# Optimization experiments

Measured on AMD Instinct MI355X. Metric: run time of the kernel, lower is better.

Reference implementation:

```python
import jax, jax.numpy as jnp
import numpy as np

TEMP = 1.0
PONDER_COST = 0.01
HALT_BIAS = 0.0


def _layernorm(x, g, b, eps=1e-5):
    mu = x.mean(-1, keepdims=True)
    var = ((x - mu) ** 2).mean(-1, keepdims=True)
    return (x - mu) * jax.lax.rsqrt(var + eps) * g + b


def _bank_forward_all(x, w1, b1, w2, b2):
    # x: [B,N,H] -> every expert's output [B,N,E,H]
    h = jax.nn.relu(jnp.einsum('bnh,ehf->bnef', x, w1) + b1)  # [B,N,E,F]
    return jnp.einsum('bnef,efh->bneh', h, w2) + b2


def setup_inputs() -> dict:
    key = jax.random.key(0)
    ks = jax.random.split(key, 10)
    B, N, H, E, F = 8, 2048, 256, 32, 512
    inv_h = 1.0 / np.sqrt(H).astype(np.float32)
    inv_f = 1.0 / np.sqrt(F).astype(np.float32)
    n = lambda k, s, sc: jax.random.normal(k, s, jnp.float32) * sc
    return {
        'tokens_in': n(ks[0], (B, N, H), 1.0),
        'Wp': n(ks[1], (H, H), inv_h), 'bp': jnp.zeros((H,), jnp.float32),
        'Wq1': n(ks[2], (H, H), inv_h), 'Wq2': n(ks[3], (H, H), inv_h),
        'keys_e': n(ks[4], (E, H), inv_h),  # torch: randn/sqrt(H)
        'transition_bias': jnp.zeros((E, E), jnp.float32),
        'halt_ln_g': jnp.ones((H,), jnp.float32), 'halt_ln_b': jnp.zeros((H,), jnp.float32),
        'halt_w': n(ks[5], (H, 1), inv_h), 'halt_b': jnp.zeros((1,), jnp.float32),
        'w1': n(ks[6], (E, H, F), inv_h), 'b1': jnp.zeros((E, F), jnp.float32),
        'w2': n(ks[7], (E, F, H), inv_f), 'b2': jnp.zeros((E, H), jnp.float32),
        'norm_g': jnp.ones((H,), jnp.float32), 'norm_b': jnp.zeros((H,), jnp.float32),
    }


def reference(tokens_in, Wp, bp, Wq1, Wq2, keys_e, transition_bias,
              halt_ln_g, halt_ln_b, halt_w, halt_b,
              w1, b1, w2, b2, norm_g, norm_b):
    H = tokens_in.shape[-1]
    scale = 1.0 / jnp.sqrt(jnp.asarray(H, tokens_in.dtype))
    tokens = tokens_in @ Wp + bp                       # input_proj [B,N,H]

    # hop 1: query-key routing + full expert bank + softmax mix
    scores_1 = ((tokens @ Wq1) @ keys_e.T) * scale     # [B,N,E]
    probs_1 = jax.nn.softmax(scores_1 / TEMP, axis=-1)
    out_1 = _bank_forward_all(tokens, w1, b1, w2, b2)  # [B,N,E,H]
    hop_1 = jnp.einsum('bneh,bne->bnh', out_1, probs_1)
    top1_idx = jnp.argmax(probs_1, axis=-1)            # [B,N]

    # halting head
    halt_prob = jax.nn.sigmoid(_layernorm(hop_1, halt_ln_g, halt_ln_b) @ halt_w + halt_b + HALT_BIAS)  # [B,N,1]

    # hop 2 with transition bias from hop-1 top expert
    scores_2 = ((hop_1 @ Wq2) @ keys_e.T) * scale + transition_bias[top1_idx]
    probs_2 = jax.nn.softmax(scores_2 / TEMP, axis=-1)
    out_2 = _bank_forward_all(hop_1, w1, b1, w2, b2)
    hop_2 = jnp.einsum('bneh,bne->bnh', out_2, probs_2)

    continue_prob = 1.0 - halt_prob
    mixed = halt_prob * hop_1 + continue_prob * hop_2
    tokens_out = _layernorm(tokens + mixed, norm_g, norm_b)
    pooled = tokens_out.mean(axis=1)                   # masked_mean (no mask)
    ponder_loss = continue_prob.mean() * PONDER_COST
    return pooled, tokens_out, ponder_loss
```

## Files before the change

### kernel.cpp

```cpp
#include <hip/hip_runtime.h>

typedef short short8 __attribute__((ext_vector_type(8)));
typedef float f32x4 __attribute__((ext_vector_type(4)));

#define MFMA16(a, b, c) __builtin_amdgcn_mfma_f32_16x16x32_bf16(a, b, c, 0, 0, 0)

static __device__ __forceinline__ unsigned pk2(float a, float b) {
  unsigned r;
  asm("v_cvt_pk_bf16_f32 %0, %1, %2" : "=v"(r) : "v"(a), "v"(b));
  return r;
}
static __device__ __forceinline__ float bf2f(unsigned short u) {
  union { unsigned u; float f; } v; v.u = ((unsigned)u) << 16; return v.f;
}
static __device__ __forceinline__ void async16(void* lds, const void* g) {
  __builtin_amdgcn_global_load_lds(
      (const __attribute__((address_space(1))) unsigned*)g,
      (__attribute__((address_space(3))) unsigned*)lds, 16, 0, 0);
}
static __device__ __forceinline__ float wsum64(float v) {
#pragma unroll
  for (int m = 1; m < 64; m <<= 1) v += __shfl_xor(v, m);
  return v;
}

#define LOAD4(B, P)                                   \
  {                                                   \
    const unsigned short* _p = (P);                   \
    B[0] = *(const short8*)(_p);                      \
    B[1] = *(const short8*)(_p + 512);                \
    B[2] = *(const short8*)(_p + 1024);               \
    B[3] = *(const short8*)(_p + 1536);               \
  }

__global__ void k_prep(const float* __restrict__ w1, const float* __restrict__ w2,
                       const float* __restrict__ Wp, const float* __restrict__ Wq1,
                       const float* __restrict__ Wq2, const float* __restrict__ keys,
                       unsigned short* __restrict__ w1f, unsigned short* __restrict__ w2f,
                       unsigned short* __restrict__ wpt, float* __restrict__ wk1,
                       float* __restrict__ wk2, float* __restrict__ dout) {
  __shared__ __align__(16) short T[64 * 266];
  const int b = blockIdx.x, tid = threadIdx.x;
  if (b < 512) {
    int e = b >> 4, fq = (b >> 2) & 3, kc = b & 3;
    const float* src = w1 + (e * 256 + kc * 64) * 512 + fq * 128;
    for (int c = tid; c < 1024; c += 256) {
      int hr = c >> 4, c8 = c & 15;
      const float* s = src + hr * 512 + c8 * 8;
      f32x4 v0 = *(const f32x4*)s;
      f32x4 v1 = *(const f32x4*)(s + 4);
      unsigned* tp = (unsigned*)(T + hr * 138 + c8 * 8);
      tp[0] = pk2(v0.x, v0.y); tp[1] = pk2(v0.z, v0.w);
      tp[2] = pk2(v1.x, v1.y); tp[3] = pk2(v1.z, v1.w);
    }
    __syncthreads();
#pragma unroll
    for (int j = 0; j < 4; ++j) {
      int o = tid + j * 256;
      int fl = o >> 3, k8 = o & 7;
      unsigned qq[4];
#pragma unroll
      for (int p = 0; p < 4; ++p) {
        unsigned a0 = (unsigned short)T[(k8 * 8 + p * 2) * 138 + fl];
        unsigned a1 = (unsigned short)T[(k8 * 8 + p * 2 + 1) * 138 + fl];
        qq[p] = a0 | (a1 << 16);
      }
      uint4 q; q.x = qq[0]; q.y = qq[1]; q.z = qq[2]; q.w = qq[3];
      int set = kc * 2 + (k8 >> 2);
      int lane = (k8 & 3) * 16 + (fl & 15);
      int wvf = fl >> 6, fr = (fl >> 4) & 3;
      *(uint4*)(w1f + (size_t)(e * 4 + fq) * 32768 + set * 4096 + wvf * 2048 + fr * 512 +
                lane * 8) = q;
    }
  } else if (b < 768) {
    int b2 = b - 512;
    int e = b2 >> 3, fq = (b2 >> 1) & 3, kcc = b2 & 1;
    const float* src = w2 + (e * 512 + fq * 128 + kcc * 64) * 256;
    for (int c = tid; c < 2048; c += 256) {
      int fr = c >> 5, c8 = c & 31;
      const float* s = src + fr * 256 + c8 * 8;
      f32x4 v0 = *(const f32x4*)s;
      f32x4 v1 = *(const f32x4*)(s + 4);
      unsigned* tp = (unsigned*)(T + fr * 266 + c8 * 8);
      tp[0] = pk2(v0.x, v0.y); tp[1] = pk2(v0.z, v0.w);
      tp[2] = pk2(v1.x, v1.y); tp[3] = pk2(v1.z, v1.w);
    }
    __syncthreads();
#pragma unroll
    for (int j = 0; j < 8; ++j) {
      int o = tid + j * 256;
      int hd = o >> 3, k8 = o & 7;
      unsigned qq[4];
#pragma unroll
      for (int p = 0; p < 4; ++p) {
        unsigned a0 = (unsigned short)T[(k8 * 8 + p * 2) * 266 + hd];
        unsigned a1 = (unsigned short)T[(k8 * 8 + p * 2 + 1) * 266 + hd];
        qq[p] = a0 | (a1 << 16);
      }
      uint4 q; q.x = qq[0]; q.y = qq[1]; q.z = qq[2]; q.w = qq[3];
      int kc2 = kcc * 2 + (k8 >> 2);
      int lane = (k8 & 3) * 16 + (hd & 15);
      *(uint4*)(w2f + (size_t)(e * 4 + fq) * 32768 + kc2 * 8192 + (hd >> 4) * 512 +
                lane * 8) = q;
    }
  } else if (b < 776) {
    int b3 = b - 768;
    int fq = b3 >> 2, kc = b3 & 3;
    const float* src = Wp + (kc * 64) * 256 + fq * 128;
    for (int c = tid; c < 1024; c += 256) {
      int hr = c >> 4, c8 = c & 15;
      const float* s = src + hr * 256 + c8 * 8;
      f32x4 v0 = *(const f32x4*)s;
      f32x4 v1 = *(const f32x4*)(s + 4);
      unsigned* tp = (unsigned*)(T + hr * 138 + c8 * 8);
      tp[0] = pk2(v0.x, v0.y); tp[1] = pk2(v0.z, v0.w);
      tp[2] = pk2(v1.x, v1.y); tp[3] = pk2(v1.z, v1.w);
    }
    __syncthreads();
#pragma unroll
    for (int j = 0; j < 4; ++j) {
      int o = tid + j * 256;
      int fl = o >> 3, k8 = o & 7;
      unsigned qq[4];
#pragma unroll
      for (int p = 0; p < 4; ++p) {
        unsigned a0 = (unsigned short)T[(k8 * 8 + p * 2) * 138 + fl];
        unsigned a1 = (unsigned short)T[(k8 * 8 + p * 2 + 1) * 138 + fl];
        qq[p] = a0 | (a1 << 16);
      }
      uint4 q; q.x = qq[0]; q.y = qq[1]; q.z = qq[2]; q.w = qq[3];
      int off = (fl * 64 + k8 * 8) ^ ((fl & 7) << 3);
      *(uint4*)(wpt + b3 * 8192 + off) = q;
    }
  } else if (b < 792) {
    int b4 = b - 776;
    const float* Wq = (b4 >= 8) ? Wq2 : Wq1;
    float* Wk = (b4 >= 8) ? wk2 : wk1;
    const int kb = (b4 & 7) * 32;
    float* KT = (float*)T;
    for (int i = tid; i < 8192; i += 256) {
      int e = i >> 8, j = i & 255;
      KT[j * 32 + ((e + j) & 31)] = keys[e * 256 + j];
    }
    __syncthreads();
    const int e = tid & 31, kk = (tid >> 5) * 2;
    f32x4 acc0 = (f32x4)(0.0f), acc1 = (f32x4)(0.0f);
    const float* wq0 = Wq + (size_t)(kb + kk) * 256;
#pragma unroll 4
    for (int j = 0; j < 256; j += 4) {
      f32x4 kt;
      kt.x = KT[j * 32 + ((e + j) & 31)];
      kt.y = KT[(j + 1) * 32 + ((e + j + 1) & 31)];
      kt.z = KT[(j + 2) * 32 + ((e + j + 2) & 31)];
      kt.w = KT[(j + 3) * 32 + ((e + j + 3) & 31)];
      acc0 += *(const f32x4*)(wq0 + j) * kt;
      acc1 += *(const f32x4*)(wq0 + 256 + j) * kt;
    }
    Wk[(kb + kk) * 32 + e] = acc0.x + acc0.y + acc0.z + acc0.w;
    Wk[(kb + kk + 1) * 32 + e] = acc1.x + acc1.y + acc1.z + acc1.w;
  } else {
    for (int i = tid; i < 2048; i += 256) dout[i] = 0.0f;
    if (tid == 0) dout[2048 + 4194304] = 0.0f;
  }
}

#define P_LDS_W 67584
#define P_LDS_BP 100352
#define P_LDS_TOT 101376

__launch_bounds__(512, 2)
__global__ void k_proj(const float* __restrict__ xin, const unsigned short* __restrict__ wpt,
                       const float* __restrict__ bp, float* __restrict__ tokf,
                       unsigned short* __restrict__ tokb) {
  extern __shared__ char smem[];
  const int tid = threadIdx.x;
  const int tb = blockIdx.x * 128;
  const int w = tid >> 6, l = tid & 63, l15 = l & 15, l4 = l >> 4;

  for (int s = tid; s < 4096; s += 512) {
    int row = s >> 5, c8 = s & 31;
    const float* src = xin + (tb + row) * 256 + c8 * 8;
    f32x4 v0 = *(const f32x4*)src;
    f32x4 v1 = *(const f32x4*)(src + 4);
    uint4 pv;
    pv.x = pk2(v0.x, v0.y); pv.y = pk2(v0.z, v0.w);
    pv.z = pk2(v1.x, v1.y); pv.w = pk2(v1.z, v1.w);
    *(uint4*)(smem + row * 528 + c8 * 16) = pv;
  }
  if (tid < 256) ((float*)(smem + P_LDS_BP))[tid] = bp[tid];
  __syncthreads();

  const int wv_f = w >> 2, wv_t = w & 3;
  for (int fq = 0; fq < 2; ++fq) {
    f32x4 acc[8];
#pragma unroll
    for (int i = 0; i < 8; ++i) acc[i] = (f32x4)(0.0f);
    const char* cbase = (const char*)(wpt + (fq * 4) * 8192);
    {
      char* dst = smem + P_LDS_W;
      async16(dst + w * 2048, cbase + w * 2048 + l * 16);
      async16(dst + w * 2048 + 1024, cbase + w * 2048 + 1024 + l * 16);
    }
    __syncthreads();
    for (int kc = 0; kc < 4; ++kc) {
      int cur = kc & 1;
      if (kc < 3) {
        char* dst = smem + P_LDS_W + (cur ^ 1) * 16384;
        const char* src = cbase + (kc + 1) * 16384;
        async16(dst + w * 2048, src + w * 2048 + l * 16);
        async16(dst + w * 2048 + 1024, src + w * 2048 + 1024 + l * 16);
      }
      const char* Wc = smem + P_LDS_W + cur * 16384;
#pragma unroll
      for (int ks = 0; ks < 2; ++ks) {
        short8 af[4], bfr[2];
#pragma unroll
        for (int fr = 0; fr < 4; ++fr) {
          int frow = wv_f * 64 + fr * 16 + l15;
          int off = (frow * 128 + ks * 64 + l4 * 16) ^ ((frow & 7) << 4);
          af[fr] = *(const short8*)(Wc + off);
        }
#pragma unroll
        for (int tf = 0; tf < 2; ++tf) {
          int tok = wv_t * 32 + tf * 16 + l15;
          bfr[tf] = *(const short8*)(smem + tok * 528 + kc * 128 + ks * 64 + l4 * 16);
        }
#pragma unroll
        for (int fr = 0; fr < 4; ++fr)
#pragma unroll
          for (int tf = 0; tf < 2; ++tf)
            acc[fr * 2 + tf] = MFMA16(af[fr], bfr[tf], acc[fr * 2 + tf]);
      }
      __syncthreads();
    }
    const float* BP = (const float*)(smem + P_LDS_BP);
#pragma unroll
    for (int fr = 0; fr < 4; ++fr) {
      int hd0 = fq * 128 + wv_f * 64 + fr * 16 + l4 * 4;
      f32x4 bv = *(const f32x4*)(BP + hd0);
#pragma unroll
      for (int tf = 0; tf < 2; ++tf) {
        int tok = tb + wv_t * 32 + tf * 16 + l15;
        f32x4 o = acc[fr * 2 + tf] + bv;
        *(f32x4*)(tokf + tok * 256 + hd0) = o;
        uint2 hv; hv.x = pk2(o.x, o.y); hv.y = pk2(o.z, o.w);
        *(uint2*)(tokb + tok * 256 + hd0) = hv;
      }
    }
  }
}

__global__ void k_router1(const float* __restrict__ tokf, const float* __restrict__ wk1,
                          float* __restrict__ probs1, int* __restrict__ top1) {
  __shared__ float WK[8192];
  const int tid = threadIdx.x;
  for (int i = tid; i < 8192; i += 256) WK[i] = wk1[i];
  __syncthreads();
  const int w = tid >> 6, l = tid & 63;
  const int e = l & 31, half = l >> 5;
  for (int tt = 0; tt < 16; ++tt) {
    int t = blockIdx.x * 64 + w * 16 + tt;
    const float* row = tokf + t * 256 + half * 128;
    const float* wkh = WK + half * 128 * 32 + e;
    float s = 0.f;
    for (int kk = 0; kk < 128; ++kk) s += row[kk] * wkh[kk * 32];
    s += __shfl_xor(s, 32);
    s *= 0.0625f;
    float m = s;
#pragma unroll
    for (int off = 16; off > 0; off >>= 1) m = fmaxf(m, __shfl_xor(m, off, 32));
    float ex = __expf(s - m);
    float sum = ex;
#pragma unroll
    for (int off = 16; off > 0; off >>= 1) sum += __shfl_xor(sum, off, 32);
    if (l < 32) probs1[t * 32 + e] = ex / sum;
    float bs = s; int bi = e;
#pragma unroll
    for (int off = 16; off > 0; off >>= 1) {
      float os = __shfl_xor(bs, off, 32);
      int oi = __shfl_xor(bi, off, 32);
      if (os > bs || (os == bs && oi < bi)) { bs = os; bi = oi; }
    }
    if (l == 0) top1[t] = bi;
  }
}

#define B_PR 65536
#define B_B1 73728
#define B_TOT 106496

__launch_bounds__(512, 2)
__global__ void k_bank(const unsigned short* __restrict__ xg, const float* __restrict__ probsg,
                       const float* __restrict__ b1g, const unsigned short* __restrict__ w1f,
                       const unsigned short* __restrict__ w2f, float* __restrict__ partg) {
  extern __shared__ char smem[];
  const int tid = threadIdx.x;
  const int xcd = blockIdx.x & 7;
  const int grp = xcd >> 2;
  const int tile = (xcd & 3) * 32 + (blockIdx.x >> 3);
  const int tb = tile * 128;
  const int w = tid >> 6, l = tid & 63, l15 = l & 15, l4 = l >> 4;
  const int wv_f = w >> 2, wv_t = w & 3;
  const int wv_h = w >> 1, wv_t2 = w & 1;
  float* PRL = (float*)(smem + B_PR);
  float* B1L = (float*)(smem + B_B1);

  for (int s = tid; s < 2048; s += 512)
    PRL[s] = probsg[(size_t)(tb + (s & 127)) * 32 + grp * 16 + (s >> 7)];
  for (int s = tid; s < 8192; s += 512) B1L[s] = b1g[grp * 8192 + s];

  short8 xr[16];
#pragma unroll
  for (int tf = 0; tf < 2; ++tf)
#pragma unroll
    for (int kc = 0; kc < 4; ++kc)
#pragma unroll
      for (int ks = 0; ks < 2; ++ks) {
        int tok = tb + wv_t * 32 + tf * 16 + l15;
        xr[tf * 8 + kc * 2 + ks] =
            *(const short8*)(xg + (size_t)tok * 256 + kc * 64 + ks * 32 + l4 * 8);
      }
  __syncthreads();

  const unsigned short* w1e = w1f + (size_t)grp * 64 * 32768;
  const unsigned short* w2e = w2f + (size_t)grp * 64 * 32768;
  const int o1 = wv_f * 2048 + l * 8;
  const int o2 = wv_h * 2048 + l * 8;

  f32x4 acc2[16];
#pragma unroll
  for (int i = 0; i < 16; ++i) acc2[i] = (f32x4)(0.0f);

  short8 wb[3][4];
  LOAD4(wb[0], w1e + 0 * 4096 + o1);
  LOAD4(wb[1], w1e + 1 * 4096 + o1);
  int hcur = 0;

  for (int el = 0; el < 64; ++el) {
    const unsigned short* w1c = w1e + (size_t)el * 32768;
    const unsigned short* w2c = w2e + (size_t)el * 32768;
    const int e = el >> 2, fq = el & 3;

    f32x4 acc1[8];
#pragma unroll
    for (int i = 0; i < 8; ++i) acc1[i] = (f32x4)(0.0f);
#pragma unroll
    for (int k = 0; k < 8; ++k) {
      if (k < 6) { LOAD4(wb[(k + 2) % 3], w1c + (k + 2) * 4096 + o1); }
      else       { LOAD4(wb[(k + 2) % 3], w2c + (k - 6) * 8192 + o2); }
      __builtin_amdgcn_s_setprio(1);
#pragma unroll
      for (int fr = 0; fr < 4; ++fr)
#pragma unroll
        for (int tf = 0; tf < 2; ++tf)
          acc1[fr * 2 + tf] = MFMA16(wb[k % 3][fr], xr[tf * 8 + k], acc1[fr * 2 + tf]);
      __builtin_amdgcn_s_setprio(0);
    }

    {
      const float* bb = B1L + e * 512 + fq * 128;
      const float* pp = PRL + e * 128;
      float p0 = pp[wv_t * 32 + l15];
      float p1 = pp[wv_t * 32 + 16 + l15];
      char* Hw = smem + hcur * 32768;
#pragma unroll
      for (int fr = 0; fr < 4; ++fr) {
        int f0 = wv_f * 64 + fr * 16 + l4 * 4;
        f32x4 bvv = *(const f32x4*)(bb + f0);
#pragma unroll
        for (int tf = 0; tf < 2; ++tf) {
          int tok = wv_t * 32 + tf * 16 + l15;
          float p = tf ? p1 : p0;
          f32x4 a = acc1[fr * 2 + tf];
          float h0 = fmaxf(a.x + bvv.x, 0.f) * p;
          float h1 = fmaxf(a.y + bvv.y, 0.f) * p;
          float h2 = fmaxf(a.z + bvv.z, 0.f) * p;
          float h3 = fmaxf(a.w + bvv.w, 0.f) * p;
          uint2 hv; hv.x = pk2(h0, h1); hv.y = pk2(h2, h3);
          *(uint2*)(Hw + ((tok * 256 + f0 * 2) ^ ((tok & 7) << 4))) = hv;
        }
      }
    }
    asm volatile("s_waitcnt lgkmcnt(0)" ::: "memory");
    __builtin_amdgcn_s_barrier();

    {
      const char* Hr = smem + hcur * 32768;
#pragma unroll
      for (int k = 8; k < 12; ++k) {
        const int t = k + 2;
        if (t < 12) { LOAD4(wb[t % 3], w2c + (t - 8) * 8192 + o2); }
        else if (el < 63) { LOAD4(wb[t % 3], w1c + 32768 + (t - 12) * 4096 + o1); }
        short8 b2f[4];
#pragma unroll
        for (int tf = 0; tf < 4; ++tf) {
          int tok = wv_t2 * 64 + tf * 16 + l15;
          b2f[tf] = *(const short8*)(
              Hr + ((tok * 256 + (k - 8) * 64 + l4 * 16) ^ ((tok & 7) << 4)));
        }
        __builtin_amdgcn_s_setprio(1);
#pragma unroll
        for (int hr = 0; hr < 4; ++hr)
#pragma unroll
          for (int tf = 0; tf < 4; ++tf)
            acc2[hr * 4 + tf] = MFMA16(wb[k % 3][hr], b2f[tf], acc2[hr * 4 + tf]);
        __builtin_amdgcn_s_setprio(0);
      }
    }
    hcur ^= 1;
  }

  float* pout = partg + (size_t)grp * 4194304;
#pragma unroll
  for (int hr = 0; hr < 4; ++hr) {
    int hd0 = wv_h * 64 + hr * 16 + l4 * 4;
#pragma unroll
    for (int tf = 0; tf < 4; ++tf) {
      int tok = tb + wv_t2 * 64 + tf * 16 + l15;
      *(f32x4*)(pout + (size_t)tok * 256 + hd0) = acc2[hr * 4 + tf];
    }
  }
}

#define M_PRB 65536
#define M_AUX 73728
#define M_TBL 106496
#define M_PSUM 110592
#define M_TOT 110656

__launch_bounds__(512)
__global__ void k_mid(const float* __restrict__ partg, const float* __restrict__ probs1,
                      const float* __restrict__ b2g, const float* __restrict__ hlg,
                      const float* __restrict__ hlb, const float* __restrict__ hwg,
                      const float* __restrict__ hbg, const float* __restrict__ wk2,
                      const float* __restrict__ tbias, const int* __restrict__ top1,
                      unsigned short* __restrict__ hop1b, float* __restrict__ haltg,
                      float* __restrict__ probs2, float* __restrict__ dout) {
  extern __shared__ char smem[];
  const int tid = threadIdx.x;
  const int tb = blockIdx.x * 64;
  float* ROWS = (float*)smem;
  float* PRB = (float*)(smem + M_PRB);
  float* AUX = (float*)(smem + M_AUX);

  for (int i = tid; i < 2048; i += 512) PRB[i] = probs1[tb * 32 + i];
  for (int i = tid; i < 8192; i += 512) AUX[i] = b2g[i];
  __syncthreads();

  for (int i = tid; i < 4096; i += 512) {
    int t = i >> 6, h4 = i & 63;
    size_t gi = (size_t)(tb + t) * 256 + h4 * 4;
    f32x4 v = *(const f32x4*)(partg + gi) + *(const f32x4*)(partg + 4194304 + gi);
    const float* pr = PRB + t * 32;
    for (int e = 0; e < 32; ++e) v += pr[e] * *(const f32x4*)(AUX + e * 256 + h4 * 4);
    *(f32x4*)(ROWS + t * 256 + h4 * 4) = v;
    uint2 hv; hv.x = pk2(v.x, v.y); hv.y = pk2(v.z, v.w);
    *(uint2*)(hop1b + gi) = hv;
  }
  __syncthreads();
  for (int i = tid; i < 8192; i += 512) AUX[i] = wk2[i];
  float* TBL = (float*)(smem + M_TBL);
  for (int i = tid; i < 1024; i += 512) TBL[i] = tbias[i];
  __syncthreads();

  const int w = tid >> 6, l = tid & 63;
  const int e = l & 31, half = l >> 5;
  float pond = 0.f;
  for (int tt = 0; tt < 8; ++tt) {
    int t = w * 8 + tt, tg = tb + t;
    const float* row = ROWS + t * 256;
    f32x4 x4 = *(const f32x4*)(row + l * 4);
    float mu = wsum64(x4.x + x4.y + x4.z + x4.w) * (1.f / 256.f);
    f32x4 d = x4 - mu;
    float var = wsum64(d.x * d.x + d.y * d.y + d.z * d.z + d.w * d.w) * (1.f / 256.f);
    float rstd = rsqrtf(var + 1e-5f);
    f32x4 g4 = *(const f32x4*)(hlg + l * 4);
    f32x4 b4 = *(const f32x4*)(hlb + l * 4);
    f32x4 w4 = *(const f32x4*)(hwg + l * 4);
    f32x4 y = d * rstd * g4 + b4;
    float z = wsum64(y.x * w4.x + y.y * w4.y + y.z * w4.z + y.w * w4.w);
    float hp = 1.f / (1.f + __expf(-(z + hbg[0])));
    if (l == 0) { haltg[tg] = hp; pond += 1.f - hp; }
    const float* rh = row + half * 128;
    const float* wkh = AUX + half * 128 * 32 + e;
    float sc = 0.f;
    for (int kk = 0; kk < 128; ++kk) sc += rh[kk] * wkh[kk * 32];
    sc += __shfl_xor(sc, 32);
    sc = sc * 0.0625f + TBL[top1[tg] * 32 + e];
    float m = sc;
#pragma unroll
    for (int off = 16; off > 0; off >>= 1) m = fmaxf(m, __shfl_xor(m, off, 32));
    float ex = __expf(sc - m);
    float sum = ex;
#pragma unroll
    for (int off = 16; off > 0; off >>= 1) sum += __shfl_xor(sum, off, 32);
    if (l < 32) probs2[tg * 32 + e] = ex / sum;
  }
  float* PS = (float*)(smem + M_PSUM);
  if (l == 0) PS[w] = pond;
  __syncthreads();
  if (tid == 0) {
    float tot = 0.f;
    for (int i = 0; i < 8; ++i) tot += PS[i];
    atomicAdd(dout + 2048 + 4194304, tot * (0.01f / 16384.f));
  }
}

#define F_PRB 65536
#define F_B2 73728
#define F_PSUM 106496
#define F_TOT 114688

__launch_bounds__(512)
__global__ void k_final(const float* __restrict__ partg, const float* __restrict__ probs2,
                        const float* __restrict__ b2g, const float* __restrict__ tokf,
                        const unsigned short* __restrict__ hop1b, const float* __restrict__ haltg,
                        const float* __restrict__ ng, const float* __restrict__ nbv,
                        float* __restrict__ dout) {
  extern __shared__ char smem[];
  const int tid = threadIdx.x;
  const int tb = blockIdx.x * 64;
  const int batch = blockIdx.x >> 5;
  float* ROWS = (float*)smem;
  float* PRB = (float*)(smem + F_PRB);
  float* B2L = (float*)(smem + F_B2);

  for (int i = tid; i < 2048; i += 512) PRB[i] = probs2[tb * 32 + i];
  for (int i = tid; i < 8192; i += 512) B2L[i] = b2g[i];
  __syncthreads();

  for (int i = tid; i < 4096; i += 512) {
    int t = i >> 6, h4 = i & 63;
    size_t gi = (size_t)(tb + t) * 256 + h4 * 4;
    f32x4 h2 = *(const f32x4*)(partg + gi) + *(const f32x4*)(partg + 4194304 + gi);
    const float* pr = PRB + t * 32;
    for (int e = 0; e < 32; ++e) h2 += pr[e] * *(const f32x4*)(B2L + e * 256 + h4 * 4);
    float hp = haltg[tb + t];
    uint2 h1v = *(const uint2*)(hop1b + gi);
    f32x4 h1;
    h1.x = bf2f(h1v.x & 0xffff); h1.y = bf2f(h1v.x >> 16);
    h1.z = bf2f(h1v.y & 0xffff); h1.w = bf2f(h1v.y >> 16);
    f32x4 tk = *(const f32x4*)(tokf + gi);
    f32x4 pre = tk + hp * h1 + (1.f - hp) * h2;
    *(f32x4*)(ROWS + t * 256 + h4 * 4) = pre;
  }
  __syncthreads();
  const int w = tid >> 6, l = tid & 63;
  f32x4 pacc = (f32x4)(0.0f);
  f32x4 g4 = *(const f32x4*)(ng + l * 4);
  f32x4 b4 = *(const f32x4*)(nbv + l * 4);
  for (int tt = 0; tt < 8; ++tt) {
    int t = w * 8 + tt, tg = tb + t;
    f32x4 x4 = *(const f32x4*)(ROWS + t * 256 + l * 4);
    float mu = wsum64(x4.x + x4.y + x4.z + x4.w) * (1.f / 256.f);
    f32x4 d = x4 - mu;
    float var = wsum64(d.x * d.x + d.y * d.y + d.z * d.z + d.w * d.w) * (1.f / 256.f);
    float rstd = rsqrtf(var + 1e-5f);
    f32x4 y = d * rstd * g4 + b4;
    *(f32x4*)(dout + 2048 + (size_t)tg * 256 + l * 4) = y;
    pacc += y;
  }
  float* PS = (float*)(smem + F_PSUM);
  *(f32x4*)(PS + w * 256 + l * 4) = pacc;
  __syncthreads();
  if (tid < 256) {
    float s = 0.f;
    for (int ww = 0; ww < 8; ++ww) s += PS[ww * 256 + tid];
    atomicAdd(dout + batch * 256 + tid, s * (1.f / 2048.f));
  }
}

extern "C" void kernel_launch(void* const* d_in, const int* in_sizes, int n_in,
                              void* d_out, int out_size, void* d_ws, size_t ws_size,
                              hipStream_t stream) {
  (void)in_sizes; (void)n_in; (void)out_size; (void)ws_size;
  const float* tokens_in = (const float*)d_in[0];
  const float* Wp = (const float*)d_in[1];
  const float* bp = (const float*)d_in[2];
  const float* Wq1 = (const float*)d_in[3];
  const float* Wq2 = (const float*)d_in[4];
  const float* keys = (const float*)d_in[5];
  const float* tbias = (const float*)d_in[6];
  const float* hlg = (const float*)d_in[7];
  const float* hlb = (const float*)d_in[8];
  const float* hw = (const float*)d_in[9];
  const float* hb = (const float*)d_in[10];
  const float* w1 = (const float*)d_in[11];
  const float* b1 = (const float*)d_in[12];
  const float* w2 = (const float*)d_in[13];
  const float* b2 = (const float*)d_in[14];
  const float* ng = (const float*)d_in[15];
  const float* nb = (const float*)d_in[16];
  float* out = (float*)d_out;
  char* ws = (char*)d_ws;

  unsigned short* w1f = (unsigned short*)(ws + 0);
  unsigned short* w2f = (unsigned short*)(ws + 8388608);
  unsigned short* wpt = (unsigned short*)(ws + 16777216);
  float* tokf = (float*)(ws + 16908288);
  unsigned short* tokb = (unsigned short*)(ws + 33685504);
  float* probs1 = (float*)(ws + 42074112);
  int* top1 = (int*)(ws + 44171264);
  unsigned short* hop1b = (unsigned short*)(ws + 44236800);
  float* haltg = (float*)(ws + 52625408);
  float* probs2 = (float*)(ws + 52690944);
  float* wk1 = (float*)(ws + 54788096);
  float* wk2 = (float*)(ws + 54820864);
  float* part = (float*)(ws + 54853632);

  k_prep<<<dim3(793), dim3(256), 0, stream>>>(w1, w2, Wp, Wq1, Wq2, keys,
                                              w1f, w2f, wpt, wk1, wk2, out);
  k_proj<<<dim3(128), dim3(512), P_LDS_TOT, stream>>>(tokens_in, wpt, bp, tokf, tokb);
  k_router1<<<dim3(256), dim3(256), 0, stream>>>(tokf, wk1, probs1, top1);
  k_bank<<<dim3(256), dim3(512), B_TOT, stream>>>(tokb, probs1, b1, w1f, w2f, part);
  k_mid<<<dim3(256), dim3(512), M_TOT, stream>>>(part, probs1, b2, hlg, hlb, hw, hb, wk2,
                                                 tbias, top1, hop1b, haltg, probs2, out);
  k_bank<<<dim3(256), dim3(512), B_TOT, stream>>>(hop1b, probs2, b1, w1f, w2f, part);
  k_final<<<dim3(256), dim3(512), F_TOT, stream>>>(part, probs2, b2, tokf, hop1b, haltg, ng, nb, out);
}
```

Before: 647.9 us.

## Switch expert bank GEMMs from 16x16x32 to 32x32x16 bf16 MFMA tiles

Reworks the expert-bank kernel to use 32x32x16 bf16 MFMA instructions instead of 16x16x32. The weight pre-swizzle kernel, the token operand loads, the hidden-activation LDS layout and swizzle, and the output store are all remapped to match the 32-lane fragment layout. Larger MFMA tiles reuse more operand data per instruction and need fewer instructions. In exchange, accumulator and register layouts change, and the new LDS swizzle may alter bank-conflict behaviour.

```diff
diff --git a/kernel.cpp b/kernel.cpp
--- a/kernel.cpp
+++ b/kernel.cpp
@@ -2,7 +2,9 @@
 
 typedef short short8 __attribute__((ext_vector_type(8)));
 typedef float f32x4 __attribute__((ext_vector_type(4)));
-
+typedef float f32x16 __attribute__((ext_vector_type(16)));
+
+#define MFMA32(a, b, c) __builtin_amdgcn_mfma_f32_32x32x16_bf16(a, b, c, 0, 0, 0)
 #define MFMA16(a, b, c) __builtin_amdgcn_mfma_f32_16x16x32_bf16(a, b, c, 0, 0, 0)
 
 static __device__ __forceinline__ unsigned pk2(float a, float b) {
@@ -57,19 +59,20 @@
 #pragma unroll
     for (int j = 0; j < 4; ++j) {
       int o = tid + j * 256;
-      int fl = o >> 3, k8 = o & 7;
+      int lane = o & 63;
+      int wvf = (o >> 6) & 1, ftile = (o >> 7) & 1, ks2 = (o >> 8) & 1, ss = (o >> 9) & 1;
+      int fl = wvf * 64 + ftile * 32 + (lane & 31);
+      int kb = ss * 32 + ks2 * 16 + ((lane >> 5) << 3);
       unsigned qq[4];
 #pragma unroll
       for (int p = 0; p < 4; ++p) {
-        unsigned a0 = (unsigned short)T[(k8 * 8 + p * 2) * 138 + fl];
-        unsigned a1 = (unsigned short)T[(k8 * 8 + p * 2 + 1) * 138 + fl];
+        unsigned a0 = (unsigned short)T[(kb + p * 2) * 138 + fl];
+        unsigned a1 = (unsigned short)T[(kb + p * 2 + 1) * 138 + fl];
         qq[p] = a0 | (a1 << 16);
       }
       uint4 q; q.x = qq[0]; q.y = qq[1]; q.z = qq[2]; q.w = qq[3];
-      int set = kc * 2 + (k8 >> 2);
-      int lane = (k8 & 3) * 16 + (fl & 15);
-      int wvf = fl >> 6, fr = (fl >> 4) & 3;
-      *(uint4*)(w1f + (size_t)(e * 4 + fq) * 32768 + set * 4096 + wvf * 2048 + fr * 512 +
+      int set = kc * 2 + ss, frag = ks2 * 2 + ftile;
+      *(uint4*)(w1f + (size_t)(e * 4 + fq) * 32768 + set * 4096 + wvf * 2048 + frag * 512 +
                 lane * 8) = q;
     }
   } else if (b < 768) {
@@ -89,18 +92,20 @@
 #pragma unroll
     for (int j = 0; j < 8; ++j) {
       int o = tid + j * 256;
-      int hd = o >> 3, k8 = o & 7;
+      int lane = o & 63;
+      int wvh = (o >> 6) & 3, htile = (o >> 8) & 1, ks2 = (o >> 9) & 1, ss = (o >> 10) & 1;
+      int hd = wvh * 64 + htile * 32 + (lane & 31);
+      int fb = ss * 32 + ks2 * 16 + ((lane >> 5) << 3);
       unsigned qq[4];
 #pragma unroll
       for (int p = 0; p < 4; ++p) {
-        unsigned a0 = (unsigned short)T[(k8 * 8 + p * 2) * 266 + hd];
-        unsigned a1 = (unsigned short)T[(k8 * 8 + p * 2 + 1) * 266 + hd];
+        unsigned a0 = (unsigned short)T[(fb + p * 2) * 266 + hd];
+        unsigned a1 = (unsigned short)T[(fb + p * 2 + 1) * 266 + hd];
         qq[p] = a0 | (a1 << 16);
       }
       uint4 q; q.x = qq[0]; q.y = qq[1]; q.z = qq[2]; q.w = qq[3];
-      int kc2 = kcc * 2 + (k8 >> 2);
-      int lane = (k8 & 3) * 16 + (hd & 15);
-      *(uint4*)(w2f + (size_t)(e * 4 + fq) * 32768 + kc2 * 8192 + (hd >> 4) * 512 +
+      int set = kcc * 2 + ss, frag = ks2 * 2 + htile;
+      *(uint4*)(w2f + (size_t)(e * 4 + fq) * 32768 + set * 8192 + wvh * 2048 + frag * 512 +
                 lane * 8) = q;
     }
   } else if (b < 776) {
@@ -299,7 +304,7 @@
   const int grp = xcd >> 2;
   const int tile = (xcd & 3) * 32 + (blockIdx.x >> 3);
   const int tb = tile * 128;
-  const int w = tid >> 6, l = tid & 63, l15 = l & 15, l4 = l >> 4;
+  const int w = tid >> 6, l = tid & 63, l31 = l & 31, l5 = l >> 5;
   const int wv_f = w >> 2, wv_t = w & 3;
   const int wv_h = w >> 1, wv_t2 = w & 1;
   float* PRL = (float*)(smem + B_PR);
@@ -310,16 +315,14 @@
   for (int s = tid; s < 8192; s += 512) B1L[s] = b1g[grp * 8192 + s];
 
   short8 xr[16];
-#pragma unroll
-  for (int tf = 0; tf < 2; ++tf)
-#pragma unroll
-    for (int kc = 0; kc < 4; ++kc)
-#pragma unroll
-      for (int ks = 0; ks < 2; ++ks) {
-        int tok = tb + wv_t * 32 + tf * 16 + l15;
-        xr[tf * 8 + kc * 2 + ks] =
-            *(const short8*)(xg + (size_t)tok * 256 + kc * 64 + ks * 32 + l4 * 8);
-      }
+  {
+    const unsigned short* xrow = xg + (size_t)(tb + wv_t * 32 + l31) * 256 + l5 * 8;
+#pragma unroll
+    for (int s = 0; s < 8; ++s)
+#pragma unroll
+      for (int ks = 0; ks < 2; ++ks)
+        xr[s * 2 + ks] = *(const short8*)(xrow + s * 32 + ks * 16);
+  }
   __syncthreads();
 
   const unsigned short* w1e = w1f + (size_t)grp * 64 * 32768;
@@ -327,9 +330,9 @@
   const int o1 = wv_f * 2048 + l * 8;
   const int o2 = wv_h * 2048 + l * 8;
 
-  f32x4 acc2[16];
-#pragma unroll
-  for (int i = 0; i < 16; ++i) acc2[i] = (f32x4)(0.0f);
+  f32x16 acc2[4];
+#pragma unroll
+  for (int i = 0; i < 4; ++i) acc2[i] = (f32x16)(0.0f);
 
   short8 wb[3][4];
   LOAD4(wb[0], w1e + 0 * 4096 + o1);
@@ -341,45 +344,41 @@
     const unsigned short* w2c = w2e + (size_t)el * 32768;
     const int e = el >> 2, fq = el & 3;
 
-    f32x4 acc1[8];
-#pragma unroll
-    for (int i = 0; i < 8; ++i) acc1[i] = (f32x4)(0.0f);
+    f32x16 acc1[2];
+#pragma unroll
+    for (int i = 0; i < 2; ++i) acc1[i] = (f32x16)(0.0f);
 #pragma unroll
     for (int k = 0; k < 8; ++k) {
       if (k < 6) { LOAD4(wb[(k + 2) % 3], w1c + (k + 2) * 4096 + o1); }
       else       { LOAD4(wb[(k + 2) % 3], w2c + (k - 6) * 8192 + o2); }
       __builtin_amdgcn_s_setprio(1);
 #pragma unroll
-      for (int fr = 0; fr < 4; ++fr)
-#pragma unroll
-        for (int tf = 0; tf < 2; ++tf)
-          acc1[fr * 2 + tf] = MFMA16(wb[k % 3][fr], xr[tf * 8 + k], acc1[fr * 2 + tf]);
+      for (int ks = 0; ks < 2; ++ks)
+#pragma unroll
+        for (int t = 0; t < 2; ++t)
+          acc1[t] = MFMA32(wb[k % 3][ks * 2 + t], xr[k * 2 + ks], acc1[t]);
       __builtin_amdgcn_s_setprio(0);
     }
 
     {
       const float* bb = B1L + e * 512 + fq * 128;
-      const float* pp = PRL + e * 128;
-      float p0 = pp[wv_t * 32 + l15];
-      float p1 = pp[wv_t * 32 + 16 + l15];
+      const float p = PRL[e * 128 + wv_t * 32 + l31];
       char* Hw = smem + hcur * 32768;
-#pragma unroll
-      for (int fr = 0; fr < 4; ++fr) {
-        int f0 = wv_f * 64 + fr * 16 + l4 * 4;
-        f32x4 bvv = *(const f32x4*)(bb + f0);
-#pragma unroll
-        for (int tf = 0; tf < 2; ++tf) {
-          int tok = wv_t * 32 + tf * 16 + l15;
-          float p = tf ? p1 : p0;
-          f32x4 a = acc1[fr * 2 + tf];
-          float h0 = fmaxf(a.x + bvv.x, 0.f) * p;
-          float h1 = fmaxf(a.y + bvv.y, 0.f) * p;
-          float h2 = fmaxf(a.z + bvv.z, 0.f) * p;
-          float h3 = fmaxf(a.w + bvv.w, 0.f) * p;
+      const int tokw = wv_t * 32 + l31;
+      const int fo = l5 * 4;
+#pragma unroll
+      for (int t = 0; t < 2; ++t)
+#pragma unroll
+        for (int q = 0; q < 4; ++q) {
+          int f0 = wv_f * 64 + t * 32 + q * 8 + fo;
+          f32x4 bvv = *(const f32x4*)(bb + f0);
+          float h0 = fmaxf(acc1[t][q * 4 + 0] + bvv.x, 0.f) * p;
+          float h1 = fmaxf(acc1[t][q * 4 + 1] + bvv.y, 0.f) * p;
+          float h2 = fmaxf(acc1[t][q * 4 + 2] + bvv.z, 0.f) * p;
+          float h3 = fmaxf(acc1[t][q * 4 + 3] + bvv.w, 0.f) * p;
           uint2 hv; hv.x = pk2(h0, h1); hv.y = pk2(h2, h3);
-          *(uint2*)(Hw + ((tok * 256 + f0 * 2) ^ ((tok & 7) << 4))) = hv;
+          *(uint2*)(Hw + ((tokw * 256 + f0 * 2) ^ ((tokw & 15) << 4))) = hv;
         }
-      }
     }
     asm volatile("s_waitcnt lgkmcnt(0)" ::: "memory");
     __builtin_amdgcn_s_barrier();
@@ -391,20 +390,24 @@
         const int t = k + 2;
         if (t < 12) { LOAD4(wb[t % 3], w2c + (t - 8) * 8192 + o2); }
         else if (el < 63) { LOAD4(wb[t % 3], w1c + 32768 + (t - 12) * 4096 + o1); }
-        short8 b2f[4];
-#pragma unroll
-        for (int tf = 0; tf < 4; ++tf) {
-          int tok = wv_t2 * 64 + tf * 16 + l15;
-          b2f[tf] = *(const short8*)(
-              Hr + ((tok * 256 + (k - 8) * 64 + l4 * 16) ^ ((tok & 7) << 4)));
+        const int s2 = k - 8;
+#pragma unroll
+        for (int ks = 0; ks < 2; ++ks) {
+          short8 b2f[2];
+#pragma unroll
+          for (int tt = 0; tt < 2; ++tt) {
+            int tokr = wv_t2 * 64 + tt * 32 + l31;
+            int fo2 = s2 * 32 + ks * 16 + l5 * 8;
+            b2f[tt] = *(const short8*)(Hr + ((tokr * 256 + fo2 * 2) ^ ((tokr & 15) << 4)));
+          }
+          __builtin_amdgcn_s_setprio(1);
+#pragma unroll
+          for (int th = 0; th < 2; ++th)
+#pragma unroll
+            for (int tt = 0; tt < 2; ++tt)
+              acc2[th * 2 + tt] = MFMA32(wb[k % 3][ks * 2 + th], b2f[tt], acc2[th * 2 + tt]);
+          __builtin_amdgcn_s_setprio(0);
         }
-        __builtin_amdgcn_s_setprio(1);
-#pragma unroll
-        for (int hr = 0; hr < 4; ++hr)
-#pragma unroll
-          for (int tf = 0; tf < 4; ++tf)
-            acc2[hr * 4 + tf] = MFMA16(wb[k % 3][hr], b2f[tf], acc2[hr * 4 + tf]);
-        __builtin_amdgcn_s_setprio(0);
       }
     }
     hcur ^= 1;
@@ -412,14 +415,21 @@
 
   float* pout = partg + (size_t)grp * 4194304;
 #pragma unroll
-  for (int hr = 0; hr < 4; ++hr) {
-    int hd0 = wv_h * 64 + hr * 16 + l4 * 4;
-#pragma unroll
-    for (int tf = 0; tf < 4; ++tf) {
-      int tok = tb + wv_t2 * 64 + tf * 16 + l15;
-      *(f32x4*)(pout + (size_t)tok * 256 + hd0) = acc2[hr * 4 + tf];
-    }
-  }
+  for (int th = 0; th < 2; ++th)
+#pragma unroll
+    for (int tt = 0; tt < 2; ++tt) {
+      int tok = tb + wv_t2 * 64 + tt * 32 + l31;
+#pragma unroll
+      for (int q = 0; q < 4; ++q) {
+        int hd0 = wv_h * 64 + th * 32 + q * 8 + l5 * 4;
+        f32x4 o;
+        o.x = acc2[th * 2 + tt][q * 4 + 0];
+        o.y = acc2[th * 2 + tt][q * 4 + 1];
+        o.z = acc2[th * 2 + tt][q * 4 + 2];
+        o.w = acc2[th * 2 + tt][q * 4 + 3];
+        *(f32x4*)(pout + (size_t)tok * 256 + hd0) = o;
+      }
+    }
 }
 
 #define M_PRB 65536
```

Measured after the change: 718.5 us. +10.9%, slower.

## Split expert bank into four expert groups with smaller 64-token blocks

Applied to the files above, without the earlier changes.

The expert-bank kernel now runs 1024 blocks of 256 threads, each covering 64 tokens and 8 experts, instead of 256 blocks of 512 threads covering 128 tokens and 16 experts. Input tokens are staged in swizzled LDS rather than held in registers, b1 is read from global memory, and the H buffer is single-buffered with an added barrier. The aim is to raise occupancy and parallelism, at the cost of doubling partial-sum traffic to four partial buffers that k_mid and k_final must read and sum, and of rereading weights more often per token.

```diff
diff --git a/kernel.cpp b/kernel.cpp
--- a/kernel.cpp
+++ b/kernel.cpp
@@ -285,45 +285,36 @@
   }
 }
 
-#define B_PR 65536
-#define B_B1 73728
-#define B_TOT 106496
-
-__launch_bounds__(512, 2)
+#define B_H 32768
+#define B_PR 49152
+#define B_TOT 51200
+
+__launch_bounds__(256, 3)
 __global__ void k_bank(const unsigned short* __restrict__ xg, const float* __restrict__ probsg,
                        const float* __restrict__ b1g, const unsigned short* __restrict__ w1f,
                        const unsigned short* __restrict__ w2f, float* __restrict__ partg) {
   extern __shared__ char smem[];
   const int tid = threadIdx.x;
   const int xcd = blockIdx.x & 7;
-  const int grp = xcd >> 2;
-  const int tile = (xcd & 3) * 32 + (blockIdx.x >> 3);
-  const int tb = tile * 128;
+  const int grp = xcd >> 1;
+  const int tile = (xcd & 1) * 128 + (blockIdx.x >> 3);
+  const int tb = tile * 64;
   const int w = tid >> 6, l = tid & 63, l15 = l & 15, l4 = l >> 4;
-  const int wv_f = w >> 2, wv_t = w & 3;
-  const int wv_h = w >> 1, wv_t2 = w & 1;
+  const int wv_f = w >> 1, wv_t = w & 1;
+  const int wv_h = w;
   float* PRL = (float*)(smem + B_PR);
-  float* B1L = (float*)(smem + B_B1);
-
-  for (int s = tid; s < 2048; s += 512)
-    PRL[s] = probsg[(size_t)(tb + (s & 127)) * 32 + grp * 16 + (s >> 7)];
-  for (int s = tid; s < 8192; s += 512) B1L[s] = b1g[grp * 8192 + s];
-
-  short8 xr[16];
-#pragma unroll
-  for (int tf = 0; tf < 2; ++tf)
-#pragma unroll
-    for (int kc = 0; kc < 4; ++kc)
-#pragma unroll
-      for (int ks = 0; ks < 2; ++ks) {
-        int tok = tb + wv_t * 32 + tf * 16 + l15;
-        xr[tf * 8 + kc * 2 + ks] =
-            *(const short8*)(xg + (size_t)tok * 256 + kc * 64 + ks * 32 + l4 * 8);
-      }
-  __syncthreads();
-
-  const unsigned short* w1e = w1f + (size_t)grp * 64 * 32768;
-  const unsigned short* w2e = w2f + (size_t)grp * 64 * 32768;
+
+  for (int s = tid; s < 2048; s += 256) {
+    int row = s >> 5, c8 = s & 31;
+    uint4 v = *(const uint4*)(xg + (size_t)(tb + row) * 256 + c8 * 8);
+    *(uint4*)(smem + ((row * 512 + c8 * 16) ^ ((row & 7) << 4))) = v;
+  }
+  for (int s = tid; s < 512; s += 256)
+    PRL[s] = probsg[(size_t)(tb + (s & 63)) * 32 + grp * 8 + (s >> 6)];
+  __syncthreads();
+
+  const unsigned short* w1e = w1f + (size_t)grp * 32 * 32768;
+  const unsigned short* w2e = w2f + (size_t)grp * 32 * 32768;
   const int o1 = wv_f * 2048 + l * 8;
   const int o2 = wv_h * 2048 + l * 8;
 
@@ -334,12 +325,12 @@
   short8 wb[3][4];
   LOAD4(wb[0], w1e + 0 * 4096 + o1);
   LOAD4(wb[1], w1e + 1 * 4096 + o1);
-  int hcur = 0;
-
-  for (int el = 0; el < 64; ++el) {
+
+  for (int el = 0; el < 32; ++el) {
     const unsigned short* w1c = w1e + (size_t)el * 32768;
     const unsigned short* w2c = w2e + (size_t)el * 32768;
     const int e = el >> 2, fq = el & 3;
+    const int eg = grp * 8 + e;
 
     f32x4 acc1[8];
 #pragma unroll
@@ -348,25 +339,32 @@
     for (int k = 0; k < 8; ++k) {
       if (k < 6) { LOAD4(wb[(k + 2) % 3], w1c + (k + 2) * 4096 + o1); }
       else       { LOAD4(wb[(k + 2) % 3], w2c + (k - 6) * 8192 + o2); }
+      short8 bfr[2];
+#pragma unroll
+      for (int tf = 0; tf < 2; ++tf) {
+        int tok = wv_t * 32 + tf * 16 + l15;
+        bfr[tf] = *(const short8*)(
+            smem + ((tok * 512 + k * 64 + l4 * 16) ^ ((tok & 7) << 4)));
+      }
       __builtin_amdgcn_s_setprio(1);
 #pragma unroll
       for (int fr = 0; fr < 4; ++fr)
 #pragma unroll
         for (int tf = 0; tf < 2; ++tf)
-          acc1[fr * 2 + tf] = MFMA16(wb[k % 3][fr], xr[tf * 8 + k], acc1[fr * 2 + tf]);
+          acc1[fr * 2 + tf] = MFMA16(wb[k % 3][fr], bfr[tf], acc1[fr * 2 + tf]);
       __builtin_amdgcn_s_setprio(0);
     }
 
+    __builtin_amdgcn_s_barrier();
+
     {
-      const float* bb = B1L + e * 512 + fq * 128;
-      const float* pp = PRL + e * 128;
-      float p0 = pp[wv_t * 32 + l15];
-      float p1 = pp[wv_t * 32 + 16 + l15];
-      char* Hw = smem + hcur * 32768;
+      const float p0 = PRL[e * 64 + wv_t * 32 + l15];
+      const float p1 = PRL[e * 64 + wv_t * 32 + 16 + l15];
+      char* Hw = smem + B_H;
 #pragma unroll
       for (int fr = 0; fr < 4; ++fr) {
         int f0 = wv_f * 64 + fr * 16 + l4 * 4;
-        f32x4 bvv = *(const f32x4*)(bb + f0);
+        f32x4 bvv = *(const f32x4*)(b1g + (size_t)eg * 512 + fq * 128 + f0);
 #pragma unroll
         for (int tf = 0; tf < 2; ++tf) {
           int tok = wv_t * 32 + tf * 16 + l15;
@@ -385,16 +383,16 @@
     __builtin_amdgcn_s_barrier();
 
     {
-      const char* Hr = smem + hcur * 32768;
+      const char* Hr = smem + B_H;
 #pragma unroll
       for (int k = 8; k < 12; ++k) {
         const int t = k + 2;
         if (t < 12) { LOAD4(wb[t % 3], w2c + (t - 8) * 8192 + o2); }
-        else if (el < 63) { LOAD4(wb[t % 3], w1c + 32768 + (t - 12) * 4096 + o1); }
+        else if (el < 31) { LOAD4(wb[t % 3], w1c + 32768 + (t - 12) * 4096 + o1); }
         short8 b2f[4];
 #pragma unroll
         for (int tf = 0; tf < 4; ++tf) {
-          int tok = wv_t2 * 64 + tf * 16 + l15;
+          int tok = tf * 16 + l15;
           b2f[tf] = *(const short8*)(
               Hr + ((tok * 256 + (k - 8) * 64 + l4 * 16) ^ ((tok & 7) << 4)));
         }
@@ -407,7 +405,6 @@
         __builtin_amdgcn_s_setprio(0);
       }
     }
-    hcur ^= 1;
   }
 
   float* pout = partg + (size_t)grp * 4194304;
@@ -416,7 +413,7 @@
     int hd0 = wv_h * 64 + hr * 16 + l4 * 4;
 #pragma unroll
     for (int tf = 0; tf < 4; ++tf) {
-      int tok = tb + wv_t2 * 64 + tf * 16 + l15;
+      int tok = tb + tf * 16 + l15;
       *(f32x4*)(pout + (size_t)tok * 256 + hd0) = acc2[hr * 4 + tf];
     }
   }
@@ -450,7 +447,8 @@
   for (int i = tid; i < 4096; i += 512) {
     int t = i >> 6, h4 = i & 63;
     size_t gi = (size_t)(tb + t) * 256 + h4 * 4;
-    f32x4 v = *(const f32x4*)(partg + gi) + *(const f32x4*)(partg + 4194304 + gi);
+    f32x4 v = *(const f32x4*)(partg + gi) + *(const f32x4*)(partg + 4194304 + gi) +
+              *(const f32x4*)(partg + 8388608 + gi) + *(const f32x4*)(partg + 12582912 + gi);
     const float* pr = PRB + t * 32;
     for (int e = 0; e < 32; ++e) v += pr[e] * *(const f32x4*)(AUX + e * 256 + h4 * 4);
     *(f32x4*)(ROWS + t * 256 + h4 * 4) = v;
@@ -532,7 +530,8 @@
   for (int i = tid; i < 4096; i += 512) {
     int t = i >> 6, h4 = i & 63;
     size_t gi = (size_t)(tb + t) * 256 + h4 * 4;
-    f32x4 h2 = *(const f32x4*)(partg + gi) + *(const f32x4*)(partg + 4194304 + gi);
+    f32x4 h2 = *(const f32x4*)(partg + gi) + *(const f32x4*)(partg + 4194304 + gi) +
+               *(const f32x4*)(partg + 8388608 + gi) + *(const f32x4*)(partg + 12582912 + gi);
     const float* pr = PRB + t * 32;
     for (int e = 0; e < 32; ++e) h2 += pr[e] * *(const f32x4*)(B2L + e * 256 + h4 * 4);
     float hp = haltg[tb + t];
@@ -612,9 +611,9 @@
                                               w1f, w2f, wpt, wk1, wk2, out);
   k_proj<<<dim3(128), dim3(512), P_LDS_TOT, stream>>>(tokens_in, wpt, bp, tokf, tokb);
   k_router1<<<dim3(256), dim3(256), 0, stream>>>(tokf, wk1, probs1, top1);
-  k_bank<<<dim3(256), dim3(512), B_TOT, stream>>>(tokb, probs1, b1, w1f, w2f, part);
+  k_bank<<<dim3(1024), dim3(256), B_TOT, stream>>>(tokb, probs1, b1, w1f, w2f, part);
   k_mid<<<dim3(256), dim3(512), M_TOT, stream>>>(part, probs1, b2, hlg, hlb, hw, hb, wk2,
                                                  tbias, top1, hop1b, haltg, probs2, out);
-  k_bank<<<dim3(256), dim3(512), B_TOT, stream>>>(hop1b, probs2, b1, w1f, w2f, part);
+  k_bank<<<dim3(1024), dim3(256), B_TOT, stream>>>(hop1b, probs2, b1, w1f, w2f, part);
   k_final<<<dim3(256), dim3(512), F_TOT, stream>>>(part, probs2, b2, tokf, hop1b, haltg, ng, nb, out);
 }
```

Result: slower. 1.942 ms (+199.8%).
